# Kernel optimization log

Measured on AMD Instinct MI355X. Metric: run time of the kernel, lower is better.

The kernel has to match this reference:

```python
import jax, jax.numpy as jnp
import numpy as np

B, N, IN_DIM, SLOT_DIM, HIDDEN = 32, 4096, 256, 256, 512
NUM_SLOTS, NUM_ITERS = 8, 3
EPS_LN = 1e-5


def layernorm(x, g, b):
    m = jnp.mean(x, axis=-1, keepdims=True)
    v = jnp.var(x, axis=-1, keepdims=True)
    return (x - m) * jax.lax.rsqrt(v + EPS_LN) * g + b


def setup_inputs() -> dict:
    key = jax.random.key(0)
    ks = jax.random.split(key, 16)
    s = 0.02
    return {
        "inputs": jax.random.normal(ks[0], (B, N, IN_DIM), jnp.float32),
        "init_noise": jax.random.normal(ks[1], (B, NUM_SLOTS, SLOT_DIM), jnp.float32),
        "mu": jax.random.normal(ks[2], (1, 1, SLOT_DIM), jnp.float32),
        "sigma_raw": jax.random.normal(ks[3], (1, 1, SLOT_DIM), jnp.float32),
        "ln_in_g": jnp.ones((IN_DIM,), jnp.float32), "ln_in_b": jnp.zeros((IN_DIM,), jnp.float32),
        "ln_s_g": jnp.ones((SLOT_DIM,), jnp.float32), "ln_s_b": jnp.zeros((SLOT_DIM,), jnp.float32),
        "ln_m_g": jnp.ones((SLOT_DIM,), jnp.float32), "ln_m_b": jnp.zeros((SLOT_DIM,), jnp.float32),
        "wq": jax.random.normal(ks[4], (SLOT_DIM, SLOT_DIM), jnp.float32) * s,
        "bq": jnp.zeros((SLOT_DIM,), jnp.float32),
        "wk": jax.random.normal(ks[5], (SLOT_DIM, IN_DIM), jnp.float32) * s,
        "bk": jnp.zeros((SLOT_DIM,), jnp.float32),
        "wv": jax.random.normal(ks[6], (SLOT_DIM, IN_DIM), jnp.float32) * s,
        "bv": jnp.zeros((SLOT_DIM,), jnp.float32),
        "w_ih": jax.random.normal(ks[7], (3 * SLOT_DIM, SLOT_DIM), jnp.float32) * s,
        "w_hh": jax.random.normal(ks[8], (3 * SLOT_DIM, SLOT_DIM), jnp.float32) * s,
        "b_ih": jnp.zeros((3 * SLOT_DIM,), jnp.float32),
        "b_hh": jnp.zeros((3 * SLOT_DIM,), jnp.float32),
        "w1": jax.random.normal(ks[9], (HIDDEN, SLOT_DIM), jnp.float32) * s,
        "b1": jnp.zeros((HIDDEN,), jnp.float32),
        "w2": jax.random.normal(ks[10], (SLOT_DIM, HIDDEN), jnp.float32) * s,
        "b2": jnp.zeros((SLOT_DIM,), jnp.float32),
    }


def gru_cell(x, h, w_ih, w_hh, b_ih, b_hh):
    # PyTorch GRUCell: gates split as (reset, update, new)
    gx = x @ w_ih.T + b_ih
    gh = h @ w_hh.T + b_hh
    xr, xz, xn = jnp.split(gx, 3, axis=-1)
    hr, hz, hn = jnp.split(gh, 3, axis=-1)
    r = jax.nn.sigmoid(xr + hr)
    z = jax.nn.sigmoid(xz + hz)
    n = jnp.tanh(xn + r * hn)
    return (1.0 - z) * n + z * h


def reference(inputs, init_noise, mu, sigma_raw, ln_in_g, ln_in_b, ln_s_g, ln_s_b,
              ln_m_g, ln_m_b, wq, bq, wk, bk, wv, bv, w_ih, w_hh, b_ih, b_hh,
              w1, b1, w2, b2):
    scale = SLOT_DIM ** (-0.5)
    x = layernorm(inputs, ln_in_g, ln_in_b)          # [B,N,Din]
    k = x @ wk.T + bk                                # [B,N,D]
    v = x @ wv.T + bv                                # [B,N,D]
    sigma = jax.nn.softplus(sigma_raw)
    slots = mu + sigma * init_noise                  # [B,S,D]
    attn = None
    for _ in range(NUM_ITERS):
        slots_prev = slots
        q = layernorm(slots, ln_s_g, ln_s_b) @ wq.T + bq      # [B,S,D]
        logits = jnp.einsum('bnd,bsd->bns', k, q) * scale     # [B,N,S]
        attn = jax.nn.softmax(logits, axis=-1) + 1e-8         # softmax over slots
        attn = attn / jnp.sum(attn, axis=1, keepdims=True)    # renorm over inputs
        updates = jnp.einsum('bnd,bns->bsd', v, attn)         # [B,S,D]
        slots = gru_cell(updates, slots_prev, w_ih, w_hh, b_ih, b_hh)
        h = jax.nn.relu(layernorm(slots, ln_m_g, ln_m_b) @ w1.T + b1)
        slots = slots + (h @ w2.T + b2)
    return slots, attn
```

## Files before the change

### kernel.cpp

```cpp
#include <hip/hip_runtime.h>
#include <hip/hip_fp16.h>
#include <cstdint>

#define DEV static __device__ __forceinline__

typedef _Float16 f16x2 __attribute__((ext_vector_type(2)));
typedef _Float16 f16x8 __attribute__((ext_vector_type(8)));
typedef float    f32x4 __attribute__((ext_vector_type(4)));

DEV float fdot2u(uint32_t a, uint32_t b, float c){
  union U { uint32_t u; f16x2 h; };
  U ua; ua.u = a; U ub; ub.u = b;
#if __has_builtin(__builtin_amdgcn_fdot2)
  return __builtin_amdgcn_fdot2(ua.h, ub.h, c, false);
#else
  return c + (float)ua.h[0]*(float)ub.h[0] + (float)ua.h[1]*(float)ub.h[1];
#endif
}

DEV float dot4(uint4 x, uint4 w, float a){
  a = fdot2u(x.x, w.x, a); a = fdot2u(x.y, w.y, a);
  a = fdot2u(x.z, w.z, a); a = fdot2u(x.w, w.w, a);
  return a;
}

DEV float wsum64(float v){
  #pragma unroll
  for (int o = 32; o; o >>= 1) v += __shfl_xor(v, o);
  return v;
}

DEV uint32_t pack2h(float a, float b){
  __half ha = __float2half(a), hb = __float2half(b);
  return (uint32_t)__half_as_ushort(ha) | ((uint32_t)__half_as_ushort(hb) << 16);
}

DEV uint32_t packsh(float v){
  float o = __shfl_xor(v, 1);
  return pack2h(v, o);
}

DEV uint4 packrow8(const float* p){
  uint4 r;
  r.x = pack2h(p[0], p[1]); r.y = pack2h(p[2], p[3]);
  r.z = pack2h(p[4], p[5]); r.w = pack2h(p[6], p[7]);
  return r;
}

DEV void gld16(const void* g, void* l){
  __builtin_amdgcn_global_load_lds(
      (const __attribute__((address_space(1))) void*)g,
      (__attribute__((address_space(3))) void*)l, 16, 0, 0);
}

__global__ __launch_bounds__(256) void k_tr(
  const float* __restrict__ wq, const float* __restrict__ wv,
  const float* __restrict__ wih, const float* __restrict__ whh,
  const float* __restrict__ w1, const float* __restrict__ w2,
  const float* __restrict__ wk,
  uint4* __restrict__ WQp4, uint4* __restrict__ WVp4,
  uint4* __restrict__ WIHp4, uint4* __restrict__ WHHp4,
  uint4* __restrict__ W1p4, uint4* __restrict__ W2p4,
  uint4* __restrict__ WKp4)
{
  int u = blockIdx.x * 256 + threadIdx.x;
  if (u < 8192){
    int e4 = u >> 8, n = u & 255;
    WVp4[u] = packrow8(wv + n*256 + 8*e4);
  } else if (u < 32768){
    int v = u - 8192; int e4 = v / 768, n = v - e4*768;
    WIHp4[v] = packrow8(wih + n*256 + 8*e4);
  } else if (u < 57344){
    int v = u - 32768; int e4 = v / 768, n = v - e4*768;
    WHHp4[v] = packrow8(whh + n*256 + 8*e4);
  } else if (u < 73728){
    int v = u - 57344; int e4 = v >> 9, n = v & 511;
    W1p4[v] = packrow8(w1 + n*256 + 8*e4);
  } else if (u < 90112){
    int v = u - 73728; int e4 = v >> 8, n = v & 255;
    W2p4[v] = packrow8(w2 + n*512 + 8*e4);
  } else if (u < 98304){
    int v = u - 90112; int e4 = v >> 8, n = v & 255;
    WQp4[v] = packrow8(wq + n*256 + 8*e4);
  } else if (u < 106496){
    int v = u - 98304; int d4 = v >> 8, c = v & 255;
    uint4 r;
    r.x = pack2h(wk[(8*d4+0)*256 + c], wk[(8*d4+1)*256 + c]);
    r.y = pack2h(wk[(8*d4+2)*256 + c], wk[(8*d4+3)*256 + c]);
    r.z = pack2h(wk[(8*d4+4)*256 + c], wk[(8*d4+5)*256 + c]);
    r.w = pack2h(wk[(8*d4+6)*256 + c], wk[(8*d4+7)*256 + c]);
    WKp4[v] = r;
  }
}

__global__ __launch_bounds__(256) void k_ln(
  const float* __restrict__ xin, const float* __restrict__ g,
  const float* __restrict__ b, uint32_t* __restrict__ xhat)
{
  int row = blockIdx.x * 4 + (threadIdx.x >> 6);
  int lane = threadIdx.x & 63;
  const float4 xv = ((const float4*)(xin + (size_t)row * 256))[lane];
  float s1 = wsum64(xv.x + xv.y + xv.z + xv.w);
  float s2 = wsum64(xv.x*xv.x + xv.y*xv.y + xv.z*xv.z + xv.w*xv.w);
  float m = s1 * (1.0f/256.0f);
  float var = s2 * (1.0f/256.0f) - m*m;
  float rstd = rsqrtf(var + 1e-5f);
  float4 gv = ((const float4*)g)[lane];
  float4 bv = ((const float4*)b)[lane];
  float y0 = (xv.x - m)*rstd*gv.x + bv.x;
  float y1 = (xv.y - m)*rstd*gv.y + bv.y;
  float y2 = (xv.z - m)*rstd*gv.z + bv.z;
  float y3 = (xv.w - m)*rstd*gv.w + bv.w;
  ((uint2*)(xhat + (size_t)row * 128))[lane] = make_uint2(pack2h(y0,y1), pack2h(y2,y3));
}

template<int MODE>
__global__ __launch_bounds__(512) void k_slot(
  const float* __restrict__ noise, const float* __restrict__ mu,
  const float* __restrict__ sigraw, float* __restrict__ S0,
  const float* __restrict__ uacc, const float* __restrict__ asum,
  const uint4* __restrict__ WVp4, const float* __restrict__ bv,
  const uint4* __restrict__ WIHp4, const uint4* __restrict__ WHHp4,
  const float* __restrict__ bih, const float* __restrict__ bhh,
  const float* __restrict__ lmg, const float* __restrict__ lmb,
  const uint4* __restrict__ W1p4, const float* __restrict__ b1,
  const uint4* __restrict__ W2p4, const float* __restrict__ b2,
  const float* __restrict__ lsg, const float* __restrict__ lsb,
  const uint4* __restrict__ WQp4, const float* __restrict__ bq,
  const uint4* __restrict__ WKp4, const float* __restrict__ bk,
  uint32_t* __restrict__ QTH, float* __restrict__ CV,
  float* __restrict__ uacc_z, float* __restrict__ asum_z)
{
  __shared__ float gx[768], gh[768];
  __shared__ float part[512];
  __shared__ uint4 hs4[32], un4[32], us4[32], sln4[32], q4[32];
  __shared__ uint4 hb4[64];
  __shared__ float redA[8], redB[8];

  const int t = threadIdx.x;
  const int h = t >> 8;
  const int c = t & 255;
  const int lane = t & 63;
  const int w8 = t >> 6;
  const int r = blockIdx.x;
  const int b = r >> 3, s = r & 7;

  float snv = 0.f, spv = 0.f;

  if (MODE == 0){
    if (t < 256){
      float x = sigraw[c];
      float sp = (x > 20.0f) ? x : log1pf(__expf(x));
      snv = mu[c] + sp * noise[r*256 + c];
      S0[r*256 + c] = snv;
    }
  } else {
    float ainv = 1.0f / asum[r];
    float hv = 0.f;
    if (t < 256){
      hv = S0[r*256 + c];
      float unv = uacc[r*256 + c] * ainv;
      uint32_t ph = packsh(hv), pu = packsh(unv);
      if (!(c & 1)){
        ((uint32_t*)hs4)[c>>1] = ph;
        ((uint32_t*)un4)[c>>1] = pu;
      }
    }
    __syncthreads();

    {
      float a = 0.f;
      #pragma unroll 8
      for (int e4 = h*16; e4 < h*16 + 16; ++e4)
        a = dot4(un4[e4], WVp4[e4*256 + c], a);
      part[t] = a;
    }
    __syncthreads();
    if (t < 256){
      float us = part[t] + part[t + 256] + bv[c];
      uint32_t p = packsh(us);
      if (!(c & 1)) ((uint32_t*)us4)[c>>1] = p;
    }
    __syncthreads();

    {
      const uint4* IN4 = h ? hs4 : us4;
      const uint4* WP = h ? WHHp4 : WIHp4;
      float a0 = 0.f, a1 = 0.f, a2 = 0.f;
      #pragma unroll 8
      for (int e4 = 0; e4 < 32; ++e4){
        uint4 x = IN4[e4];
        a0 = dot4(x, WP[e4*768 + c], a0);
        a1 = dot4(x, WP[e4*768 + 256 + c], a1);
        a2 = dot4(x, WP[e4*768 + 512 + c], a2);
      }
      float* OUT = h ? gh : gx;
      OUT[c] = a0; OUT[256 + c] = a1; OUT[512 + c] = a2;
    }
    __syncthreads();

    if (t < 256){
      float xr = gx[c]     + bih[c];
      float xz = gx[256+c] + bih[256+c];
      float xn = gx[512+c] + bih[512+c];
      float hr = gh[c]     + bhh[c];
      float hz = gh[256+c] + bhh[256+c];
      float hn = gh[512+c] + bhh[512+c];
      float rg = 1.f/(1.f + __expf(-(xr + hr)));
      float zg = 1.f/(1.f + __expf(-(xz + hz)));
      float ng = tanhf(xn + rg*hn);
      spv = (1.f - zg)*ng + zg*hv;
      float a = wsum64(spv), bs = wsum64(spv*spv);
      if (lane == 0){ redA[w8] = a; redB[w8] = bs; }
    }
    __syncthreads();
    {
      float s1 = redA[0]+redA[1]+redA[2]+redA[3];
      float s2 = redB[0]+redB[1]+redB[2]+redB[3];
      float m = s1*(1.f/256.f), var = s2*(1.f/256.f) - m*m;
      float rstd = rsqrtf(var + 1e-5f);
      if (t < 256){
        float slv = (spv - m)*rstd*lmg[c] + lmb[c];
        uint32_t p = packsh(slv);
        if (!(c & 1)) ((uint32_t*)sln4)[c>>1] = p;
      }
    }
    __syncthreads();

    {
      float a = 0.f;
      #pragma unroll 8
      for (int e4 = 0; e4 < 32; ++e4)
        a = dot4(sln4[e4], W1p4[e4*512 + t], a);
      float hval = fmaxf(a + b1[t], 0.f);
      float o = __shfl_xor(hval, 1);
      if (!(t & 1)) ((uint32_t*)hb4)[t>>1] = pack2h(hval, o);
    }
    __syncthreads();

    {
      float a = 0.f;
      #pragma unroll 8
      for (int e4 = h*32; e4 < h*32 + 32; ++e4)
        a = dot4(hb4[e4], W2p4[e4*256 + c], a);
      part[t] = a;
    }
    __syncthreads();
    if (t < 256){
      snv = spv + part[t] + part[t + 256] + b2[c];
      S0[r*256 + c] = snv;
    }
  }

  if (MODE != 2){
    if (t < 256){
      float a = wsum64(snv), bs = wsum64(snv*snv);
      if (lane == 0){ redA[w8] = a; redB[w8] = bs; }
    }
    __syncthreads();
    {
      float s1 = redA[0]+redA[1]+redA[2]+redA[3];
      float s2 = redB[0]+redB[1]+redB[2]+redB[3];
      float m = s1*(1.f/256.f), var = s2*(1.f/256.f) - m*m;
      float rstd = rsqrtf(var + 1e-5f);
      if (t < 256){
        float slv = (snv - m)*rstd*lsg[c] + lsb[c];
        uint32_t p = packsh(slv);
        if (!(c & 1)) ((uint32_t*)sln4)[c>>1] = p;
      }
    }
    __syncthreads();

    {
      float a = 0.f;
      #pragma unroll 8
      for (int e4 = h*16; e4 < h*16 + 16; ++e4)
        a = dot4(sln4[e4], WQp4[e4*256 + c], a);
      part[t] = a;
    }
    __syncthreads();
    if (t < 256){
      float qv = part[t] + part[t + 256] + bq[c];
      float p = wsum64(bk[c] * qv);
      if (lane == 0) redA[w8] = p;
      uint32_t pk = packsh(qv);
      if (!(c & 1)) ((uint32_t*)q4)[c>>1] = pk;
    }
    __syncthreads();
    {
      float cv = redA[0]+redA[1]+redA[2]+redA[3];
      if (t == 0) CV[r] = cv;
    }

    {
      float a = 0.f;
      #pragma unroll 8
      for (int e4 = h*16; e4 < h*16 + 16; ++e4)
        a = dot4(q4[e4], WKp4[e4*256 + c], a);
      part[t] = a;
    }
    __syncthreads();
    if (t < 256){
      float qtv = part[t] + part[t + 256];
      uint32_t p = packsh(qtv);
      if (!(c & 1)) QTH[b*1024 + (c>>1)*8 + s] = p;
      uacc_z[r*256 + c] = 0.f;
    }
    if (t == 0) asum_z[r] = 0.f;
  }
}

template<bool LAST>
__global__ __launch_bounds__(256) void k_attn(
  const uint32_t* __restrict__ xhat,
  const uint32_t* __restrict__ qtpk, const float* __restrict__ cvec,
  float* __restrict__ uacc, float* __restrict__ asum,
  float* __restrict__ attn_out)
{
  __shared__ uint32_t xs[8192];
  __shared__ uint32_t qs[1024];
  __shared__ float attn_lds[64][16];
  __shared__ float up_lds[8][256];

  const int b = blockIdx.y, chunk = blockIdx.x;
  const int t = threadIdx.x;
  const int l = t & 63, w = t >> 6;
  const int g = l >> 4, sl = l & 15;

  for (int i = t; i < 1024; i += 256) qs[i] = qtpk[b*1024 + i];

  auto stage = [&](int st){
    const size_t gr0 = (size_t)b*4096 + (size_t)chunk*256 + st*64;
    #pragma unroll
    for (int i = 0; i < 8; ++i){
      int n  = w*8 + i;
      int rl = 2*n + (l >> 5);
      int ql = (l & 31) ^ (rl & 7);
      gld16(xhat + (gr0 + rl)*128 + ql*4, xs + n*256);
    }
  };

  stage(0);
  __syncthreads();

  uint4 bq[8];
  #pragma unroll
  for (int kk = 0; kk < 8; ++kk){
    if (sl < 8){
      uint4 v;
      v.x = qs[(16*kk + 4*g + 0)*8 + sl];
      v.y = qs[(16*kk + 4*g + 1)*8 + sl];
      v.z = qs[(16*kk + 4*g + 2)*8 + sl];
      v.w = qs[(16*kk + 4*g + 3)*8 + sl];
      bq[kk] = v;
    } else bq[kk] = make_uint4(0u,0u,0u,0u);
  }
  const float cv = (sl < 8) ? cvec[b*8 + sl] : 0.f;

  float up[8][4];
  #pragma unroll
  for (int s = 0; s < 8; ++s){ up[s][0]=0.f; up[s][1]=0.f; up[s][2]=0.f; up[s][3]=0.f; }
  float asl_acc = 0.f;

  for (int st = 0; st < 4; ++st){
    if (st){ __syncthreads(); stage(st); __syncthreads(); }
    const int L0 = 16*w;

    f32x4 acc; acc[0]=0.f; acc[1]=0.f; acc[2]=0.f; acc[3]=0.f;
    const int rowA = L0 + sl;
    #pragma unroll
    for (int kk = 0; kk < 8; ++kk){
      uint4 av = *(const uint4*)(xs + rowA*128 + (((4*kk + g) ^ (rowA & 7)) << 2));
      union { uint4 u; f16x8 h; } A, B;
      A.u = av; B.u = bq[kk];
      acc = __builtin_amdgcn_mfma_f32_16x16x32_f16(A.h, B.h, acc, 0, 0, 0);
    }

    #pragma unroll
    for (int reg = 0; reg < 4; ++reg){
      float d = (acc[reg] + cv) * 0.0625f;
      float m = d;
      m = fmaxf(m, __shfl_xor(m, 1));
      m = fmaxf(m, __shfl_xor(m, 2));
      m = fmaxf(m, __shfl_xor(m, 4));
      float e = __expf(d - m);
      float ssum = e;
      ssum += __shfl_xor(ssum, 1);
      ssum += __shfl_xor(ssum, 2);
      ssum += __shfl_xor(ssum, 4);
      float a = e / ssum + 1e-8f;
      asl_acc += a;
      attn_lds[L0 + 4*g + reg][sl] = a;
    }

    #pragma unroll 4
    for (int rr = 0; rr < 16; ++rr){
      const int row = L0 + rr;
      const uint32_t* xp = xs + row*128 + ((((l>>1) ^ (row & 7)) << 2) | ((l & 1) << 1));
      uint2 xv = *(const uint2*)xp;
      float x0 = __half2float(__ushort_as_half((unsigned short)(xv.x & 0xffff)));
      float x1 = __half2float(__ushort_as_half((unsigned short)(xv.x >> 16)));
      float x2 = __half2float(__ushort_as_half((unsigned short)(xv.y & 0xffff)));
      float x3 = __half2float(__ushort_as_half((unsigned short)(xv.y >> 16)));
      const float4 a0 = *(const float4*)&attn_lds[row][0];
      const float4 a1 = *(const float4*)&attn_lds[row][4];
      float as8[8] = {a0.x, a0.y, a0.z, a0.w, a1.x, a1.y, a1.z, a1.w};
      #pragma unroll
      for (int s = 0; s < 8; ++s){
        up[s][0] += as8[s]*x0; up[s][1] += as8[s]*x1;
        up[s][2] += as8[s]*x2; up[s][3] += as8[s]*x3;
      }
    }

    if (LAST){
      __syncthreads();
      const size_t gr0 = (size_t)b*4096 + (size_t)chunk*256 + st*64;
      int row = t >> 2, s0 = (t & 3)*2;
      float2 v = *(const float2*)&attn_lds[row][s0];
      *(float2*)(attn_out + (gr0 + row)*8 + s0) = v;
    }
  }

  {
    float v = asl_acc;
    v += __shfl_xor(v, 16);
    v += __shfl_xor(v, 32);
    if (l < 8) atomicAdd(&asum[b*8 + l], v);
  }

  __syncthreads();
  #pragma unroll
  for (int ww = 0; ww < 4; ++ww){
    if (w == ww){
      #pragma unroll
      for (int s = 0; s < 8; ++s){
        float4* dst = (float4*)&up_lds[s][l*4];
        float4 v = make_float4(up[s][0], up[s][1], up[s][2], up[s][3]);
        if (ww){ float4 o = *dst; v.x += o.x; v.y += o.y; v.z += o.z; v.w += o.w; }
        *dst = v;
      }
    }
    __syncthreads();
  }
  #pragma unroll
  for (int s = 0; s < 8; ++s)
    atomicAdd(&uacc[(b*8 + s)*256 + t], up_lds[s][t]);
}

__global__ __launch_bounds__(256) void k_out(
  const float* __restrict__ S0, const float* __restrict__ asum,
  float* __restrict__ out)
{
  int i = blockIdx.x * 256 + threadIdx.x;
  if (i < 65536) out[i] = S0[i];
  else {
    int j = i - 65536;
    int b = j >> 15;
    int s = j & 7;
    out[i] = out[i] * (1.0f / asum[b*8 + s]);
  }
}

extern "C" void kernel_launch(void* const* d_in, const int* in_sizes, int n_in,
                              void* d_out, int out_size, void* d_ws, size_t ws_size,
                              hipStream_t stream) {
  const float* inputs = (const float*)d_in[0];
  const float* noise  = (const float*)d_in[1];
  const float* mu     = (const float*)d_in[2];
  const float* sigraw = (const float*)d_in[3];
  const float* lng    = (const float*)d_in[4];
  const float* lnb    = (const float*)d_in[5];
  const float* lsg    = (const float*)d_in[6];
  const float* lsb    = (const float*)d_in[7];
  const float* lmg    = (const float*)d_in[8];
  const float* lmb    = (const float*)d_in[9];
  const float* wq     = (const float*)d_in[10];
  const float* bq     = (const float*)d_in[11];
  const float* wk     = (const float*)d_in[12];
  const float* bk     = (const float*)d_in[13];
  const float* wv     = (const float*)d_in[14];
  const float* bv     = (const float*)d_in[15];
  const float* wih    = (const float*)d_in[16];
  const float* whh    = (const float*)d_in[17];
  const float* bih    = (const float*)d_in[18];
  const float* bhh    = (const float*)d_in[19];
  const float* w1     = (const float*)d_in[20];
  const float* b1     = (const float*)d_in[21];
  const float* w2     = (const float*)d_in[22];
  const float* b2     = (const float*)d_in[23];
  float* out = (float*)d_out;

  char* w = (char*)d_ws;
  size_t o = 0;
  uint32_t* XH = (uint32_t*)w;  o += 67108864;
  uint32_t* QT = (uint32_t*)(w + o); o += 131072;
  float* CV  = (float*)(w + o); o += 1024;
  float* UA  = (float*)(w + o); o += 262144;
  float* AS  = (float*)(w + o); o += 1024;
  float* S0  = (float*)(w + o); o += 262144;
  uint4* WQp = (uint4*)(w + o); o += 131072;
  uint4* WVp = (uint4*)(w + o); o += 131072;
  uint4* WIHp= (uint4*)(w + o); o += 393216;
  uint4* WHHp= (uint4*)(w + o); o += 393216;
  uint4* W1p = (uint4*)(w + o); o += 262144;
  uint4* W2p = (uint4*)(w + o); o += 262144;
  uint4* WKp = (uint4*)(w + o); o += 131072;

  k_tr<<<416, 256, 0, stream>>>(wq, wv, wih, whh, w1, w2, wk,
                                WQp, WVp, WIHp, WHHp, W1p, W2p, WKp);
  k_ln<<<32768, 256, 0, stream>>>(inputs, lng, lnb, XH);
  k_slot<0><<<256, 512, 0, stream>>>(noise, mu, sigraw, S0, UA, AS,
      WVp, bv, WIHp, WHHp, bih, bhh, lmg, lmb, W1p, b1, W2p, b2,
      lsg, lsb, WQp, bq, WKp, bk, QT, CV, UA, AS);

  dim3 ga(16, 32);
  for (int it = 0; it < 3; ++it){
    if (it == 2) k_attn<true ><<<ga, 256, 0, stream>>>(XH, QT, CV, UA, AS, out + 65536);
    else         k_attn<false><<<ga, 256, 0, stream>>>(XH, QT, CV, UA, AS, out + 65536);
    if (it < 2)
      k_slot<1><<<256, 512, 0, stream>>>(noise, mu, sigraw, S0, UA, AS,
          WVp, bv, WIHp, WHHp, bih, bhh, lmg, lmb, W1p, b1, W2p, b2,
          lsg, lsb, WQp, bq, WKp, bk, QT, CV, UA, AS);
    else
      k_slot<2><<<256, 512, 0, stream>>>(noise, mu, sigraw, S0, UA, AS,
          WVp, bv, WIHp, WHHp, bih, bhh, lmg, lmb, W1p, b1, W2p, b2,
          lsg, lsb, WQp, bq, WKp, bk, QT, CV, UA, AS);
  }
  k_out<<<4352, 256, 0, stream>>>(S0, AS, out);
}
```

Baseline: 383.2 us.

## Fuse LN and weight packing, register-prefetch x tiles, replace atomics with partials

Merges the weight-pack and input layernorm kernels into one launch. In the attention kernel, async global-to-LDS loads are replaced by register-staged prefetch of the next 64-row tile, overlapped with the current tile's compute, and occupancy is hinted with launch_bounds(256,2). The float atomics into the update and attention-sum accumulators become per-chunk partial buffers that the slot kernel reduces, which also removes the zeroing step. The last slot kernel writes slots straight to the output so the copy in k_out is dropped. This costs 16x more partial-buffer traffic and more registers held for staging.

```diff
diff --git a/kernel.cpp b/kernel.cpp
--- a/kernel.cpp
+++ b/kernel.cpp
@@ -47,13 +47,9 @@
   return r;
 }
 
-DEV void gld16(const void* g, void* l){
-  __builtin_amdgcn_global_load_lds(
-      (const __attribute__((address_space(1))) void*)g,
-      (__attribute__((address_space(3))) void*)l, 16, 0, 0);
-}
-
-__global__ __launch_bounds__(256) void k_tr(
+__global__ __launch_bounds__(256) void k_lntr(
+  const float* __restrict__ xin, const float* __restrict__ lng,
+  const float* __restrict__ lnb, uint32_t* __restrict__ xhat,
   const float* __restrict__ wq, const float* __restrict__ wv,
   const float* __restrict__ wih, const float* __restrict__ whh,
   const float* __restrict__ w1, const float* __restrict__ w2,
@@ -63,40 +59,37 @@
   uint4* __restrict__ W1p4, uint4* __restrict__ W2p4,
   uint4* __restrict__ WKp4)
 {
-  int u = blockIdx.x * 256 + threadIdx.x;
-  if (u < 8192){
-    int e4 = u >> 8, n = u & 255;
-    WVp4[u] = packrow8(wv + n*256 + 8*e4);
-  } else if (u < 32768){
-    int v = u - 8192; int e4 = v / 768, n = v - e4*768;
-    WIHp4[v] = packrow8(wih + n*256 + 8*e4);
-  } else if (u < 57344){
-    int v = u - 32768; int e4 = v / 768, n = v - e4*768;
-    WHHp4[v] = packrow8(whh + n*256 + 8*e4);
-  } else if (u < 73728){
-    int v = u - 57344; int e4 = v >> 9, n = v & 511;
-    W1p4[v] = packrow8(w1 + n*256 + 8*e4);
-  } else if (u < 90112){
-    int v = u - 73728; int e4 = v >> 8, n = v & 255;
-    W2p4[v] = packrow8(w2 + n*512 + 8*e4);
-  } else if (u < 98304){
-    int v = u - 90112; int e4 = v >> 8, n = v & 255;
-    WQp4[v] = packrow8(wq + n*256 + 8*e4);
-  } else if (u < 106496){
-    int v = u - 98304; int d4 = v >> 8, c = v & 255;
-    uint4 r;
-    r.x = pack2h(wk[(8*d4+0)*256 + c], wk[(8*d4+1)*256 + c]);
-    r.y = pack2h(wk[(8*d4+2)*256 + c], wk[(8*d4+3)*256 + c]);
-    r.z = pack2h(wk[(8*d4+4)*256 + c], wk[(8*d4+5)*256 + c]);
-    r.w = pack2h(wk[(8*d4+6)*256 + c], wk[(8*d4+7)*256 + c]);
-    WKp4[v] = r;
-  }
-}
-
-__global__ __launch_bounds__(256) void k_ln(
-  const float* __restrict__ xin, const float* __restrict__ g,
-  const float* __restrict__ b, uint32_t* __restrict__ xhat)
-{
+  if (blockIdx.x >= 32768){
+    int u = (blockIdx.x - 32768) * 256 + threadIdx.x;
+    if (u < 8192){
+      int e4 = u >> 8, n = u & 255;
+      WVp4[u] = packrow8(wv + n*256 + 8*e4);
+    } else if (u < 32768){
+      int v = u - 8192; int e4 = v / 768, n = v - e4*768;
+      WIHp4[v] = packrow8(wih + n*256 + 8*e4);
+    } else if (u < 57344){
+      int v = u - 32768; int e4 = v / 768, n = v - e4*768;
+      WHHp4[v] = packrow8(whh + n*256 + 8*e4);
+    } else if (u < 73728){
+      int v = u - 57344; int e4 = v >> 9, n = v & 511;
+      W1p4[v] = packrow8(w1 + n*256 + 8*e4);
+    } else if (u < 90112){
+      int v = u - 73728; int e4 = v >> 8, n = v & 255;
+      W2p4[v] = packrow8(w2 + n*512 + 8*e4);
+    } else if (u < 98304){
+      int v = u - 90112; int e4 = v >> 8, n = v & 255;
+      WQp4[v] = packrow8(wq + n*256 + 8*e4);
+    } else if (u < 106496){
+      int v = u - 98304; int d4 = v >> 8, c = v & 255;
+      uint4 r;
+      r.x = pack2h(wk[(8*d4+0)*256 + c], wk[(8*d4+1)*256 + c]);
+      r.y = pack2h(wk[(8*d4+2)*256 + c], wk[(8*d4+3)*256 + c]);
+      r.z = pack2h(wk[(8*d4+4)*256 + c], wk[(8*d4+5)*256 + c]);
+      r.w = pack2h(wk[(8*d4+6)*256 + c], wk[(8*d4+7)*256 + c]);
+      WKp4[v] = r;
+    }
+    return;
+  }
   int row = blockIdx.x * 4 + (threadIdx.x >> 6);
   int lane = threadIdx.x & 63;
   const float4 xv = ((const float4*)(xin + (size_t)row * 256))[lane];
@@ -105,8 +98,8 @@
   float m = s1 * (1.0f/256.0f);
   float var = s2 * (1.0f/256.0f) - m*m;
   float rstd = rsqrtf(var + 1e-5f);
-  float4 gv = ((const float4*)g)[lane];
-  float4 bv = ((const float4*)b)[lane];
+  float4 gv = ((const float4*)lng)[lane];
+  float4 bv = ((const float4*)lnb)[lane];
   float y0 = (xv.x - m)*rstd*gv.x + bv.x;
   float y1 = (xv.y - m)*rstd*gv.y + bv.y;
   float y2 = (xv.z - m)*rstd*gv.z + bv.z;
@@ -117,8 +110,10 @@
 template<int MODE>
 __global__ __launch_bounds__(512) void k_slot(
   const float* __restrict__ noise, const float* __restrict__ mu,
-  const float* __restrict__ sigraw, float* __restrict__ S0,
-  const float* __restrict__ uacc, const float* __restrict__ asum,
+  const float* __restrict__ sigraw,
+  const float* S0, float* SDST,
+  const float* __restrict__ UAp, const float* __restrict__ ASp,
+  float* __restrict__ AS,
   const uint4* __restrict__ WVp4, const float* __restrict__ bv,
   const uint4* __restrict__ WIHp4, const uint4* __restrict__ WHHp4,
   const float* __restrict__ bih, const float* __restrict__ bhh,
@@ -128,8 +123,7 @@
   const float* __restrict__ lsg, const float* __restrict__ lsb,
   const uint4* __restrict__ WQp4, const float* __restrict__ bq,
   const uint4* __restrict__ WKp4, const float* __restrict__ bk,
-  uint32_t* __restrict__ QTH, float* __restrict__ CV,
-  float* __restrict__ uacc_z, float* __restrict__ asum_z)
+  uint32_t* __restrict__ QTH, float* __restrict__ CV)
 {
   __shared__ float gx[768], gh[768];
   __shared__ float part[512];
@@ -152,14 +146,26 @@
       float x = sigraw[c];
       float sp = (x > 20.0f) ? x : log1pf(__expf(x));
       snv = mu[c] + sp * noise[r*256 + c];
-      S0[r*256 + c] = snv;
+      SDST[r*256 + c] = snv;
     }
   } else {
-    float ainv = 1.0f / asum[r];
+    if (w8 == 0){
+      float v = (lane < 16) ? ASp[lane*256 + r] : 0.f;
+      v += __shfl_xor(v, 1); v += __shfl_xor(v, 2);
+      v += __shfl_xor(v, 4); v += __shfl_xor(v, 8);
+      if (lane == 0) redA[0] = v;
+    }
+    __syncthreads();
+    const float asum_r = redA[0];
+    if (MODE == 2 && t == 0) AS[r] = asum_r;
+    const float ainv = 1.0f / asum_r;
     float hv = 0.f;
     if (t < 256){
       hv = S0[r*256 + c];
-      float unv = uacc[r*256 + c] * ainv;
+      float us = 0.f;
+      #pragma unroll
+      for (int ch = 0; ch < 16; ++ch) us += UAp[ch*65536 + r*256 + c];
+      float unv = us * ainv;
       uint32_t ph = packsh(hv), pu = packsh(unv);
       if (!(c & 1)){
         ((uint32_t*)hs4)[c>>1] = ph;
@@ -248,7 +254,7 @@
     __syncthreads();
     if (t < 256){
       snv = spv + part[t] + part[t + 256] + b2[c];
-      S0[r*256 + c] = snv;
+      SDST[r*256 + c] = snv;
     }
   }
 
@@ -304,43 +310,44 @@
       float qtv = part[t] + part[t + 256];
       uint32_t p = packsh(qtv);
       if (!(c & 1)) QTH[b*1024 + (c>>1)*8 + s] = p;
-      uacc_z[r*256 + c] = 0.f;
-    }
-    if (t == 0) asum_z[r] = 0.f;
+    }
   }
 }
 
 template<bool LAST>
-__global__ __launch_bounds__(256) void k_attn(
+__global__ __launch_bounds__(256, 2) void k_attn(
   const uint32_t* __restrict__ xhat,
   const uint32_t* __restrict__ qtpk, const float* __restrict__ cvec,
-  float* __restrict__ uacc, float* __restrict__ asum,
+  float* __restrict__ UAp, float* __restrict__ ASp,
   float* __restrict__ attn_out)
 {
   __shared__ uint32_t xs[8192];
   __shared__ uint32_t qs[1024];
   __shared__ float attn_lds[64][16];
   __shared__ float up_lds[8][256];
+  __shared__ float as_red[4][8];
 
   const int b = blockIdx.y, chunk = blockIdx.x;
   const int t = threadIdx.x;
   const int l = t & 63, w = t >> 6;
   const int g = l >> 4, sl = l & 15;
 
+  const size_t base = (size_t)b*4096 + (size_t)chunk*256;
+
+  uint4 stg[8];
+  #pragma unroll
+  for (int i = 0; i < 8; ++i){
+    int c16 = i*256 + t;
+    int row = c16 >> 5, q = c16 & 31;
+    stg[i] = *(const uint4*)(xhat + (base + row)*128 + q*4);
+  }
   for (int i = t; i < 1024; i += 256) qs[i] = qtpk[b*1024 + i];
-
-  auto stage = [&](int st){
-    const size_t gr0 = (size_t)b*4096 + (size_t)chunk*256 + st*64;
-    #pragma unroll
-    for (int i = 0; i < 8; ++i){
-      int n  = w*8 + i;
-      int rl = 2*n + (l >> 5);
-      int ql = (l & 31) ^ (rl & 7);
-      gld16(xhat + (gr0 + rl)*128 + ql*4, xs + n*256);
-    }
-  };
-
-  stage(0);
+  #pragma unroll
+  for (int i = 0; i < 8; ++i){
+    int c16 = i*256 + t;
+    int row = c16 >> 5, q = c16 & 31;
+    *(uint4*)(xs + row*128 + ((q ^ (row & 7)) << 2)) = stg[i];
+  }
   __syncthreads();
 
   uint4 bq[8];
@@ -363,7 +370,6 @@
   float asl_acc = 0.f;
 
   for (int st = 0; st < 4; ++st){
-    if (st){ __syncthreads(); stage(st); __syncthreads(); }
     const int L0 = 16*w;
 
     f32x4 acc; acc[0]=0.f; acc[1]=0.f; acc[2]=0.f; acc[3]=0.f;
@@ -391,6 +397,16 @@
       float a = e / ssum + 1e-8f;
       asl_acc += a;
       attn_lds[L0 + 4*g + reg][sl] = a;
+    }
+
+    if (st < 3){
+      const size_t g2 = base + (size_t)(st+1)*64;
+      #pragma unroll
+      for (int i = 0; i < 8; ++i){
+        int c16 = i*256 + t;
+        int row = c16 >> 5, q = c16 & 31;
+        stg[i] = *(const uint4*)(xhat + (g2 + row)*128 + q*4);
+      }
     }
 
     #pragma unroll 4
@@ -414,10 +430,20 @@
 
     if (LAST){
       __syncthreads();
-      const size_t gr0 = (size_t)b*4096 + (size_t)chunk*256 + st*64;
       int row = t >> 2, s0 = (t & 3)*2;
       float2 v = *(const float2*)&attn_lds[row][s0];
-      *(float2*)(attn_out + (gr0 + row)*8 + s0) = v;
+      *(float2*)(attn_out + (base + (size_t)st*64 + row)*8 + s0) = v;
+    }
+
+    if (st < 3){
+      __syncthreads();
+      #pragma unroll
+      for (int i = 0; i < 8; ++i){
+        int c16 = i*256 + t;
+        int row = c16 >> 5, q = c16 & 31;
+        *(uint4*)(xs + row*128 + ((q ^ (row & 7)) << 2)) = stg[i];
+      }
+      __syncthreads();
     }
   }
 
@@ -425,7 +451,7 @@
     float v = asl_acc;
     v += __shfl_xor(v, 16);
     v += __shfl_xor(v, 32);
-    if (l < 8) atomicAdd(&asum[b*8 + l], v);
+    if (l < 8) as_red[w][l] = v;
   }
 
   __syncthreads();
@@ -444,21 +470,18 @@
   }
   #pragma unroll
   for (int s = 0; s < 8; ++s)
-    atomicAdd(&uacc[(b*8 + s)*256 + t], up_lds[s][t]);
+    UAp[(size_t)chunk*65536 + (size_t)(b*8 + s)*256 + t] = up_lds[s][t];
+  if (t < 8)
+    ASp[chunk*256 + b*8 + t] = as_red[0][t] + as_red[1][t] + as_red[2][t] + as_red[3][t];
 }
 
 __global__ __launch_bounds__(256) void k_out(
-  const float* __restrict__ S0, const float* __restrict__ asum,
-  float* __restrict__ out)
+  const float* __restrict__ AS, float* __restrict__ out)
 {
-  int i = blockIdx.x * 256 + threadIdx.x;
-  if (i < 65536) out[i] = S0[i];
-  else {
-    int j = i - 65536;
-    int b = j >> 15;
-    int s = j & 7;
-    out[i] = out[i] * (1.0f / asum[b*8 + s]);
-  }
+  int j = blockIdx.x * 256 + threadIdx.x;
+  int b = j >> 15;
+  int s = j & 7;
+  out[65536 + j] = out[65536 + j] * (1.0f / AS[b*8 + s]);
 }
 
 extern "C" void kernel_launch(void* const* d_in, const int* in_sizes, int n_in,
@@ -495,7 +518,6 @@
   uint32_t* XH = (uint32_t*)w;  o += 67108864;
   uint32_t* QT = (uint32_t*)(w + o); o += 131072;
   float* CV  = (float*)(w + o); o += 1024;
-  float* UA  = (float*)(w + o); o += 262144;
   float* AS  = (float*)(w + o); o += 1024;
   float* S0  = (float*)(w + o); o += 262144;
   uint4* WQp = (uint4*)(w + o); o += 131072;
@@ -505,26 +527,28 @@
   uint4* W1p = (uint4*)(w + o); o += 262144;
   uint4* W2p = (uint4*)(w + o); o += 262144;
   uint4* WKp = (uint4*)(w + o); o += 131072;
-
-  k_tr<<<416, 256, 0, stream>>>(wq, wv, wih, whh, w1, w2, wk,
-                                WQp, WVp, WIHp, WHHp, W1p, W2p, WKp);
-  k_ln<<<32768, 256, 0, stream>>>(inputs, lng, lnb, XH);
-  k_slot<0><<<256, 512, 0, stream>>>(noise, mu, sigraw, S0, UA, AS,
+  float* UAp = (float*)(w + o); o += 4194304;
+  float* ASp = (float*)(w + o); o += 16384;
+
+  k_lntr<<<33184, 256, 0, stream>>>(inputs, lng, lnb, XH,
+                                    wq, wv, wih, whh, w1, w2, wk,
+                                    WQp, WVp, WIHp, WHHp, W1p, W2p, WKp);
+  k_slot<0><<<256, 512, 0, stream>>>(noise, mu, sigraw, S0, S0, UAp, ASp, AS,
       WVp, bv, WIHp, WHHp, bih, bhh, lmg, lmb, W1p, b1, W2p, b2,
-      lsg, lsb, WQp, bq, WKp, bk, QT, CV, UA, AS);
+      lsg, lsb, WQp, bq, WKp, bk, QT, CV);
 
   dim3 ga(16, 32);
   for (int it = 0; it < 3; ++it){
-    if (it == 2) k_attn<true ><<<ga, 256, 0, stream>>>(XH, QT, CV, UA, AS, out + 65536);
-    else         k_attn<false><<<ga, 256, 0, stream>>>(XH, QT, CV, UA, AS, out + 65536);
+    if (it == 2) k_attn<true ><<<ga, 256, 0, stream>>>(XH, QT, CV, UAp, ASp, out + 65536);
+    else         k_attn<false><<<ga, 256, 0, stream>>>(XH, QT, CV, UAp, ASp, out + 65536);
     if (it < 2)
-      k_slot<1><<<256, 512, 0, stream>>>(noise, mu, sigraw, S0, UA, AS,
+      k_slot<1><<<256, 512, 0, stream>>>(noise, mu, sigraw, S0, S0, UAp, ASp, AS,
           WVp, bv, WIHp, WHHp, bih, bhh, lmg, lmb, W1p, b1, W2p, b2,
-          lsg, lsb, WQp, bq, WKp, bk, QT, CV, UA, AS);
+          lsg, lsb, WQp, bq, WKp, bk, QT, CV);
     else
-      k_slot<2><<<256, 512, 0, stream>>>(noise, mu, sigraw, S0, UA, AS,
+      k_slot<2><<<256, 512, 0, stream>>>(noise, mu, sigraw, S0, out, UAp, ASp, AS,
           WVp, bv, WIHp, WHHp, bih, bhh, lmg, lmb, W1p, b1, W2p, b2,
-          lsg, lsb, WQp, bq, WKp, bk, QT, CV, UA, AS);
-  }
-  k_out<<<4352, 256, 0, stream>>>(S0, AS, out);
-}
+          lsg, lsb, WQp, bq, WKp, bk, QT, CV);
+  }
+  k_out<<<4096, 256, 0, stream>>>(AS, out);
+}
```

Result: slower. 410.6 us (+7.1%).
